# Performance work log

Hardware: AMD Instinct MI355X
Metric: run time of the kernel (lower is better)

The kernel has to match this reference:

```python
import jax, jax.numpy as jnp
import numpy as np

V, D, F, H, NB, S, B = 16384, 512, 2048, 8, 4, 512, 2
T_STEPS = 3      # config.T: number of PC inference iterations
GAMMA = 0.1      # state-update step size


def _layernorm(x, s, b):
    m = x.mean(-1, keepdims=True)
    v = ((x - m) ** 2).mean(-1, keepdims=True)
    return (x - m) * jax.lax.rsqrt(v + 1e-5) * s + b


def setup_inputs() -> dict:
    key = jax.random.key(0)
    ks = jax.random.split(key, 12)
    r = lambda k, sh: jax.random.normal(k, sh, jnp.float32) * 0.02
    return {
        'word_emb': r(ks[0], (V, D)),
        'pos_emb': r(ks[1], (S, D)),
        'Wq': r(ks[2], (NB, D, D)),
        'Wk': r(ks[3], (NB, D, D)),
        'Wv': r(ks[4], (NB, D, D)),
        'bq': jnp.zeros((NB, D), jnp.float32),
        'bk': jnp.zeros((NB, D), jnp.float32),
        'bv': jnp.zeros((NB, D), jnp.float32),
        'Wo': r(ks[5], (NB, D, D)),
        'bo': jnp.zeros((NB, D), jnp.float32),
        'ln1_s': jnp.ones((NB, D), jnp.float32),
        'ln1_b': jnp.zeros((NB, D), jnp.float32),
        'ln2_s': jnp.ones((NB, D), jnp.float32),
        'ln2_b': jnp.zeros((NB, D), jnp.float32),
        'W1': r(ks[6], (NB, D, F)),
        'b1': jnp.zeros((NB, F), jnp.float32),
        'W2': r(ks[7], (NB, F, D)),
        'b2': jnp.zeros((NB, D), jnp.float32),
        'Wout': r(ks[8], (D, V)),
        'bout': jnp.zeros((V,), jnp.float32),
        'input_ids': jax.random.randint(ks[9], (B, S), 0, V),
        'target_ids': jax.random.randint(ks[10], (B, S), 0, V),
    }


def _forward(word_emb, pos_emb, Wq, Wk, Wv, bq, bk, bv, Wo, bo,
             ln1_s, ln1_b, ln2_s, ln2_b, W1, b1, W2, b2, Wout, bout,
             input_ids, target_ids):
    Bsz, Sl = input_ids.shape
    dh = D // H
    scale = 1.0 / float(np.sqrt(dh))
    ids = jnp.clip(input_ids, 0, V - 1)
    target = jax.nn.one_hot(jnp.clip(target_ids, 0, V - 1), V, dtype=word_emb.dtype)
    # bottom prediction: word + position embeddings
    mu_emb = word_emb[ids] + pos_emb[jnp.arange(Sl)][None]  # (B,S,D)
    causal = jnp.tril(jnp.ones((Sl, Sl), bool))
    neg = jnp.finfo(word_emb.dtype).min

    def attn(x, b):
        h = _layernorm(x, ln1_s[b], ln1_b[b])
        q = (h @ Wq[b] + bq[b]).reshape(Bsz, Sl, H, dh)
        k = (h @ Wk[b] + bk[b]).reshape(Bsz, Sl, H, dh)
        v = (h @ Wv[b] + bv[b]).reshape(Bsz, Sl, H, dh)
        sc = jnp.einsum('bqhd,bkhd->bhqk', q, k) * scale
        sc = jnp.where(causal, sc, neg)
        a = jax.nn.softmax(sc, axis=-1)
        return jnp.einsum('bhqk,bkhd->bqhd', a, v).reshape(Bsz, Sl, D)

    # generative functions g[l]: x_l -> mu_{l+1}; 4 PC layers per block
    # (pc_qkv->attn ctx, pc_output->Wo, pc_layer1->gelu(fc1), pc_layer2->fc2)
    gs = []
    for b in range(NB):
        gs.append(lambda x, b=b: attn(x, b))
        gs.append(lambda x, b=b: x @ Wo[b] + bo[b])
        gs.append(lambda x, b=b: jax.nn.gelu(_layernorm(x, ln2_s[b], ln2_b[b]) @ W1[b] + b1[b]))
        gs.append(lambda x, b=b: x @ W2[b] + b2[b])
    g_top = lambda x: x @ Wout + bout  # output pc layer -> logits mu

    # init_x: forward sweep sets each latent to its prediction
    xs = [mu_emb]
    for g in gs:
        xs.append(g(xs[-1]))
    L = len(gs)

    # T-step iterative PC inference: eps_l = x_l - mu_l, top clamped to target
    # x_l <- x_l + GAMMA * (J_{g_l}(x_l)^T eps_{l+1} - eps_l)
    for _ in range(T_STEPS):
        preds, vjps = [], []
        for l in range(L):
            mu, vj = jax.vjp(gs[l], xs[l])
            preds.append(mu)
            vjps.append(vj)
        logits, vj_top = jax.vjp(g_top, xs[L])
        eps = [xs[0] - mu_emb] + [xs[l + 1] - preds[l] for l in range(L)]
        eps_top = logits - target
        new_xs = []
        for l in range(L + 1):
            td = vjps[l](eps[l + 1])[0] if l < L else vj_top(eps_top)[0]
            new_xs.append(xs[l] + GAMMA * (td - eps[l]))
        xs = new_xs

    return g_top(xs[L])  # get_mu('linear_output')


def reference(word_emb, pos_emb, Wq, Wk, Wv, bq, bk, bv, Wo, bo,
              ln1_s, ln1_b, ln2_s, ln2_b, W1, b1, W2, b2, Wout, bout,
              input_ids, target_ids):
    return _forward(word_emb, pos_emb, Wq, Wk, Wv, bq, bk, bv, Wo, bo,
                    ln1_s, ln1_b, ln2_s, ln2_b, W1, b1, W2, b2, Wout, bout,
                    input_ids, target_ids)
```

## Files before the change

kernel.cpp:

```cpp
#include <hip/hip_runtime.h>
#include <hip/hip_bf16.h>
#include <math.h>

#define D_   512
#define F_   2048
#define V_   16384
#define H_   8
#define DH_  64
#define S_   512
#define B_   2
#define M_   1024
#define MD_  (M_ * D_)
#define MF_  (M_ * F_)
#define GAMMA_ 0.1f

typedef unsigned int u32;
typedef unsigned short u16;
typedef __attribute__((ext_vector_type(4))) float f32x4;
typedef __attribute__((ext_vector_type(8))) short s16x8;
typedef __attribute__((ext_vector_type(4))) u16 u16x4;
typedef __attribute__((ext_vector_type(8))) u16 u16x8;

__device__ __forceinline__ u16 f2b(float f) {
    __hip_bfloat16 h = __float2bfloat16(f);
    return *reinterpret_cast<u16*>(&h);
}
__device__ __forceinline__ float b2f(u16 v) {
    u32 u = ((u32)v) << 16;
    float f; __builtin_memcpy(&f, &u, 4); return f;
}
__device__ __forceinline__ u16x4 pack4(f32x4 v) {
    u16x4 o; o.x = f2b(v[0]); o.y = f2b(v[1]); o.z = f2b(v[2]); o.w = f2b(v[3]);
    return o;
}

__device__ __forceinline__ void gl_lds16(const void* g, void* l) {
    __builtin_amdgcn_global_load_lds((const __attribute__((address_space(1))) u32*)g,
                                     (__attribute__((address_space(3))) u32*)l, 16, 0, 0);
}

__device__ __forceinline__ float gelu_f(float v) {
    float u = 0.7978845608028654f * (v + 0.044715f * v * v * v);
    return 0.5f * v * (1.f + tanhf(u));
}

__device__ __forceinline__ f32x4 xpose4(f32x4 v, int b) {
#pragma unroll
    for (int s = 1; s < 4; s <<= 1) {
        f32x4 nv;
#pragma unroll
        for (int j = 0; j < 4; ++j) {
            float ex = __shfl_xor(v[j ^ s], s, 64);
            nv[j] = ((b ^ j) & s) ? ex : v[j];
        }
        v = nv;
    }
    return v;
}

__device__ __forceinline__ float wave_sum(float v) {
#pragma unroll
    for (int o = 32; o > 0; o >>= 1) v += __shfl_xor(v, o, 64);
    return v;
}

#define E_F32   0
#define E_GELU  1
#define E_TD    2
#define E_EC2   3
#define E_QKV3  4
#define E_OUT   5
#define E_BF16  6

template<int BK>
__device__ __forceinline__ int swz(int c, int row) {
    if constexpr (BK == 32) return c ^ ((row >> 1) & 3);
    else                    return c ^ (row & 7);
}

template<int BM, int BN, int BK, int FM, int FN, int EPI>
__global__ __launch_bounds__(256)
void mfma_gemm(const u16* __restrict__ A, const u16* __restrict__ B,
               float* __restrict__ Cf, u16* __restrict__ Cb,
               u16* __restrict__ Cb2, u16* __restrict__ Cb3,
               const float* __restrict__ bias,
               int K, int lda, int ldb, int ldc,
               long sC, long sKz, float alpha,
               const float* __restrict__ base, const float* __restrict__ subv,
               const float* __restrict__ cvec, const u16* __restrict__ woutTb,
               const int* __restrict__ tcl,
               float* __restrict__ ebF, u16* __restrict__ ebB)
{
    constexpr int WC = BN / (FN * 16);
    static_assert((BM / (FM * 16)) * WC == 4, "4 waves");
    constexpr int LPR = BK / 8;
    constexpr int RPI = 2048 / BK;
    constexpr int NISS = BM / RPI + BN / RPI;
    __shared__ __align__(16) u16 Asl[3][BM * BK];
    __shared__ __align__(16) u16 Bsl[3][BN * BK];
    const int t = threadIdx.x, l = t & 63, wid = t >> 6;
    const int m0 = blockIdx.y * BM, n0 = blockIdx.x * BN;
    const long z = blockIdx.z;
    A += z * sKz;
    B += z * sKz;
    if (Cf) Cf += z * sC;

    f32x4 acc[FM][FN] = {};
    const int rm = (wid / WC) * (FM * 16), cn = (wid % WC) * (FN * 16);
    const int lr = l & 15, hi = l >> 4;
    const int srl = t / LPR, sc = t % LPR;

    auto stage = [&](int k0, int pb) {
#pragma unroll
        for (int i = 0; i < BM / RPI; ++i) {
            int row = i * RPI + srl;
            gl_lds16(A + (size_t)(m0 + row) * lda + k0 + swz<BK>(sc, row) * 8,
                     &Asl[pb][i * 2048 + t * 8]);
        }
#pragma unroll
        for (int i = 0; i < BN / RPI; ++i) {
            int row = i * RPI + srl;
            gl_lds16(B + (size_t)(n0 + row) * ldb + k0 + swz<BK>(sc, row) * 8,
                     &Bsl[pb][i * 2048 + t * 8]);
        }
    };
    auto compute = [&](int pb) {
#pragma unroll
        for (int kk = 0; kk < BK / 32; ++kk) {
            s16x8 av[FM], bv[FN];
#pragma unroll
            for (int fm = 0; fm < FM; ++fm)
                av[fm] = *(const s16x8*)&Asl[pb][(rm + fm * 16 + lr) * BK + swz<BK>(kk * 4 + hi, lr) * 8];
#pragma unroll
            for (int fn = 0; fn < FN; ++fn)
                bv[fn] = *(const s16x8*)&Bsl[pb][(cn + fn * 16 + lr) * BK + swz<BK>(kk * 4 + hi, lr) * 8];
#pragma unroll
            for (int fm = 0; fm < FM; ++fm)
#pragma unroll
                for (int fn = 0; fn < FN; ++fn)
                    acc[fm][fn] = __builtin_amdgcn_mfma_f32_16x16x32_bf16(av[fm], bv[fn], acc[fm][fn], 0, 0, 0);
        }
    };

    const int nst = K / BK;
    stage(0, 0);
    if (nst > 1) stage(BK, 1);
    int rd = 0, wr = 2;
    for (int s = 0; s < nst; ++s) {
        if (s < nst - 1)
            asm volatile("s_waitcnt vmcnt(%0)" :: "i"(NISS) : "memory");
        else
            asm volatile("s_waitcnt vmcnt(0)" ::: "memory");
        __builtin_amdgcn_s_barrier();
        __builtin_amdgcn_sched_barrier(0);
        compute(rd);
        if (s + 2 < nst) stage((s + 2) * BK, wr);
        rd = (rd + 1 == 3) ? 0 : rd + 1;
        wr = (wr + 1 == 3) ? 0 : wr + 1;
    }

    const int qb = lr & 3, qi = lr >> 2;
#pragma unroll
    for (int fm = 0; fm < FM; ++fm)
#pragma unroll
        for (int fn = 0; fn < FN; ++fn) {
            const int gm = m0 + rm + fm * 16 + hi * 4 + qb;
            const int gn0 = n0 + cn + fn * 16 + qi * 4;
            const size_t idx0 = (size_t)gm * ldc + gn0;
            if constexpr (EPI == E_QKV3) {
                const int gnf = n0 + cn + fn * 16;
                const int sel = gnf >> 9;
                if (sel < 2) {
                    f32x4 v = xpose4(acc[fm][fn], qb);
                    f32x4 bv4 = *(const f32x4*)&bias[gn0];
#pragma unroll
                    for (int j = 0; j < 4; ++j) v[j] += bv4[j];
                    int b = gm >> 9, s = gm & (S_ - 1);
                    int d9 = gn0 & 511, h = d9 >> 6, d = d9 & 63;
                    u16* dst = (sel == 0) ? Cb : Cb2;
                    *(u16x4*)&dst[(((size_t)(b * H_ + h) * S_ + s) << 6) + d] = pack4(v);
                } else {
                    const int gnl = gnf + lr;
                    const int gm0 = m0 + rm + fm * 16 + hi * 4;
                    int b = gm0 >> 9, s0 = gm0 & (S_ - 1);
                    int d9 = gnl & 511, h = d9 >> 6, d = d9 & 63;
                    float bb = bias[gnl];
                    f32x4 v = acc[fm][fn];
#pragma unroll
                    for (int j = 0; j < 4; ++j) v[j] += bb;
                    *(u16x4*)&Cb3[((((size_t)(b * H_ + h)) << 6) + d) * S_ + s0] = pack4(v);
                }
            } else {
                f32x4 v = xpose4(acc[fm][fn], qb);
                if constexpr (EPI == E_F32) {
#pragma unroll
                    for (int j = 0; j < 4; ++j) v[j] *= alpha;
                    if (bias) {
                        f32x4 bv4 = *(const f32x4*)&bias[gn0];
#pragma unroll
                        for (int j = 0; j < 4; ++j) v[j] += bv4[j];
                    }
                    *(f32x4*)&Cf[idx0] = v;
                    if (Cb) *(u16x4*)&Cb[idx0] = pack4(v);
                } else if constexpr (EPI == E_OUT) {
                    f32x4 bv4 = *(const f32x4*)&bias[gn0];
#pragma unroll
                    for (int j = 0; j < 4; ++j) v[j] += bv4[j];
                    *(f32x4*)&Cf[idx0] = v;
                } else if constexpr (EPI == E_GELU) {
                    f32x4 bv4 = *(const f32x4*)&bias[gn0];
#pragma unroll
                    for (int j = 0; j < 4; ++j) v[j] = gelu_f(v[j] + bv4[j]);
                    *(u16x4*)&Cb[idx0] = pack4(v);
                } else if constexpr (EPI == E_TD) {
                    const int tc = tcl[gm];
                    f32x4 cv4 = *(const f32x4*)&cvec[gn0];
                    f32x4 ba4 = *(const f32x4*)&base[idx0];
                    u16x4 gv = *(const u16x4*)&woutTb[(size_t)tc * D_ + gn0];
                    f32x4 dlt, o2;
#pragma unroll
                    for (int j = 0; j < 4; ++j)
                        dlt[j] = GAMMA_ * (v[j] + cv4[j] - b2f(gv[j]));
                    if (subv) {
                        f32x4 sv4 = *(const f32x4*)&subv[idx0];
#pragma unroll
                        for (int j = 0; j < 4; ++j) dlt[j] -= GAMMA_ * sv4[j];
                    }
#pragma unroll
                    for (int j = 0; j < 4; ++j) o2[j] = ba4[j] + dlt[j];
                    if (Cf) *(f32x4*)&Cf[idx0] = o2;
                    *(u16x4*)&Cb[idx0] = pack4(o2);
                    if (ebF) *(f32x4*)&ebF[idx0] = dlt;
                    if (ebB) *(u16x4*)&ebB[idx0] = pack4(dlt);
                } else if constexpr (EPI == E_EC2) {
                    f32x4 ba4 = *(const f32x4*)&base[idx0];
                    f32x4 sv4 = *(const f32x4*)&subv[idx0];
#pragma unroll
                    for (int j = 0; j < 4; ++j) v[j] = ba4[j] - sv4[j] - GAMMA_ * v[j];
                    *(f32x4*)&Cf[idx0] = v;
                } else if constexpr (EPI == E_BF16) {
                    *(u16x4*)&Cb[idx0] = pack4(v);
                }
            }
        }
}

__global__ __launch_bounds__(128)
void flash_attn(const u16* __restrict__ q, const u16* __restrict__ k,
                const u16* __restrict__ vT, u16* __restrict__ ctx)
{
    __shared__ __align__(16) u16 Ks[3][64 * 64];
    __shared__ __align__(16) u16 Vs[3][64 * 64];
    __shared__ __align__(16) u16 Ps[2][16 * 64];
    const int t = threadIdx.x, l = t & 63, w = t >> 6;
    const int qt = blockIdx.x, z = blockIdx.y;
    const int bb = z >> 3, hh = z & 7;
    const int lr = l & 15, hi = l >> 4;
    const u16* qp = q + (((size_t)z * S_ + qt * 32 + w * 16) << 6);
    const u16* kp = k + ((size_t)z * S_ << 6);
    const u16* vp = vT + (((size_t)z) << 6) * S_;

    const s16x8 aq0 = *(const s16x8*)&qp[lr * 64 + hi * 8];
    const s16x8 aq1 = *(const s16x8*)&qp[lr * 64 + 32 + hi * 8];

    f32x4 o[4] = {};
    float m[4], ls[4];
#pragma unroll
    for (int r = 0; r < 4; ++r) { m[r] = -3.0e38f; ls[r] = 0.f; }
    const int qrow = qt * 32 + w * 16 + hi * 4;
    const int srow = t >> 3, scl = t & 7;
    const int cg = (scl ^ (srow & 7)) * 8;
    const int sw7 = (lr & 7);
    const int jmax = qt >> 1;

    auto stage = [&](int j, int pb) {
#pragma unroll
        for (int i = 0; i < 4; ++i)
            gl_lds16(kp + ((size_t)(j * 64 + i * 16 + srow) << 6) + cg,
                     &Ks[pb][i * 1024 + t * 8]);
#pragma unroll
        for (int i = 0; i < 4; ++i)
            gl_lds16(vp + (size_t)(i * 16 + srow) * S_ + j * 64 + cg,
                     &Vs[pb][i * 1024 + t * 8]);
    };

    stage(0, 0);
    if (jmax > 0) stage(1, 1);
    int rd = 0, wr = 2;
    for (int j = 0; j <= jmax; ++j) {
        if (j < jmax) asm volatile("s_waitcnt vmcnt(8)" ::: "memory");
        else          asm volatile("s_waitcnt vmcnt(0)" ::: "memory");
        __builtin_amdgcn_s_barrier();
        __builtin_amdgcn_sched_barrier(0);

        float pv[4][4];
#pragma unroll
        for (int fn = 0; fn < 4; ++fn) {
            f32x4 acc = {};
            acc = __builtin_amdgcn_mfma_f32_16x16x32_bf16(aq0,
                    *(const s16x8*)&Ks[rd][((fn * 16 + lr) << 6) + ((hi ^ sw7) * 8)], acc, 0, 0, 0);
            acc = __builtin_amdgcn_mfma_f32_16x16x32_bf16(aq1,
                    *(const s16x8*)&Ks[rd][((fn * 16 + lr) << 6) + (((hi + 4) ^ sw7) * 8)], acc, 0, 0, 0);
#pragma unroll
            for (int r = 0; r < 4; ++r) pv[fn][r] = acc[r] * 0.125f;
        }
        if (j == jmax) {
#pragma unroll
            for (int fn = 0; fn < 4; ++fn) {
                int col = j * 64 + fn * 16 + lr;
#pragma unroll
                for (int r = 0; r < 4; ++r)
                    if (col > qrow + r) pv[fn][r] = -3.0e38f;
            }
        }
        float sc[4], rs[4];
#pragma unroll
        for (int r = 0; r < 4; ++r) {
            float x = fmaxf(fmaxf(pv[0][r], pv[1][r]), fmaxf(pv[2][r], pv[3][r]));
#pragma unroll
            for (int off = 1; off < 16; off <<= 1) x = fmaxf(x, __shfl_xor(x, off, 64));
            float nm = fmaxf(m[r], x);
            sc[r] = expf(m[r] - nm);
            m[r] = nm;
            rs[r] = 0.f;
        }
#pragma unroll
        for (int fn = 0; fn < 4; ++fn)
#pragma unroll
            for (int r = 0; r < 4; ++r) {
                float p = expf(pv[fn][r] - m[r]);
                pv[fn][r] = p;
                rs[r] += p;
            }
#pragma unroll
        for (int r = 0; r < 4; ++r) {
#pragma unroll
            for (int off = 1; off < 16; off <<= 1) rs[r] += __shfl_xor(rs[r], off, 64);
            ls[r] = ls[r] * sc[r] + rs[r];
        }
#pragma unroll
        for (int fn = 0; fn < 4; ++fn)
#pragma unroll
            for (int r = 0; r < 4; ++r) o[fn][r] *= sc[r];
#pragma unroll
        for (int fn = 0; fn < 4; ++fn)
#pragma unroll
            for (int r = 0; r < 4; ++r) {
                int qr = hi * 4 + r;
                int ci = (2 * fn + (lr >> 3)) ^ (qr & 7);
                Ps[w][qr * 64 + ci * 8 + (lr & 7)] = f2b(pv[fn][r]);
            }
#pragma unroll
        for (int ks = 0; ks < 2; ++ks) {
            const s16x8 pa = *(const s16x8*)&Ps[w][lr * 64 + (((4 * ks + hi) ^ sw7) * 8)];
#pragma unroll
            for (int fn = 0; fn < 4; ++fn)
                o[fn] = __builtin_amdgcn_mfma_f32_16x16x32_bf16(pa,
                        *(const s16x8*)&Vs[rd][((fn * 16 + lr) << 6) + (((hi + 4 * ks) ^ sw7) * 8)], o[fn], 0, 0, 0);
        }
        if (j + 2 <= jmax) stage(j + 2, wr);
        rd = (rd + 1 == 3) ? 0 : rd + 1;
        wr = (wr + 1 == 3) ? 0 : wr + 1;
    }
    float inv[4];
#pragma unroll
    for (int r = 0; r < 4; ++r) inv[r] = 1.f / ls[r];
    u16* cp = ctx + ((size_t)(bb * S_ + qt * 32 + w * 16) * D_) + hh * 64;
    const int qb = lr & 3, qi = lr >> 2;
#pragma unroll
    for (int fn = 0; fn < 4; ++fn) {
        f32x4 v = o[fn];
#pragma unroll
        for (int r = 0; r < 4; ++r) v[r] *= inv[r];
        v = xpose4(v, qb);
        *(u16x4*)&cp[(size_t)(hi * 4 + qb) * D_ + fn * 16 + qi * 4] = pack4(v);
    }
}

__global__ __launch_bounds__(256)
void mega_prep(const float* __restrict__ Wq, const float* __restrict__ Wk,
               const float* __restrict__ Wv, const float* __restrict__ Wo,
               const float* __restrict__ W1, const float* __restrict__ W2,
               const float* __restrict__ Wout,
               const float* __restrict__ bq, const float* __restrict__ bk,
               const float* __restrict__ bv, const int* __restrict__ target_ids,
               u16* __restrict__ wqkvT, u16* __restrict__ woT, u16* __restrict__ w1T,
               u16* __restrict__ w2T, u16* __restrict__ woutT,
               u16* __restrict__ woutD, float* __restrict__ qkvb, int* __restrict__ tcl)
{
    __shared__ float tile[64][65];
    const int g = blockIdx.x, t = threadIdx.x;

    const float* in = nullptr;
    u16 *outT = nullptr, *outC = nullptr;
    int R = 512, C = 512, tx = 0, ty = 0;

    if (g < 768) {
        int sel = g / 256, rem = g % 256, zz = rem >> 6, tl = rem & 63;
        in = (sel == 0 ? Wq : sel == 1 ? Wk : Wv) + (size_t)zz * 262144;
        outT = wqkvT + (size_t)zz * 786432 + sel * 262144;
        tx = tl & 7; ty = tl >> 3;
    } else if (g < 1024) {
        int rem = g - 768, zz = rem >> 6, tl = rem & 63;
        in = Wo + (size_t)zz * 262144; outT = woT + (size_t)zz * 262144;
        tx = tl & 7; ty = tl >> 3;
    } else if (g < 2048) {
        int rem = g - 1024, zz = rem >> 8, tl = rem & 255;
        in = W1 + (size_t)zz * 1048576; outT = w1T + (size_t)zz * 1048576;
        C = 2048; tx = tl & 31; ty = tl >> 5;
    } else if (g < 3072) {
        int rem = g - 2048, zz = rem >> 8, tl = rem & 255;
        in = W2 + (size_t)zz * 1048576; outT = w2T + (size_t)zz * 1048576;
        R = 2048; tx = tl & 7; ty = tl >> 3;
    } else if (g < 5120) {
        int tl = g - 3072;
        in = Wout; outT = woutT; outC = woutD;
        C = 16384; tx = tl & 255; ty = tl >> 8;
    } else {
        for (int i = t; i < M_; i += 256) {
            int v = target_ids[i];
            tcl[i] = v < 0 ? 0 : (v > V_ - 1 ? V_ - 1 : v);
        }
        for (int i = t; i < 4 * 1536; i += 256) {
            int b = i / 1536, j = i - b * 1536;
            qkvb[i] = (j < 512) ? bq[b * 512 + j]
                    : (j < 1024) ? bk[b * 512 + j - 512] : bv[b * 512 + j - 1024];
        }
        return;
    }

    const int r0 = ty * 64, c0 = tx * 64;
#pragma unroll
    for (int p = 0; p < 4; ++p) {
        int row = p * 16 + (t >> 4), col = (t & 15) * 4;
        float4 v = *(const float4*)&in[(size_t)(r0 + row) * C + c0 + col];
        tile[row][col] = v.x; tile[row][col + 1] = v.y;
        tile[row][col + 2] = v.z; tile[row][col + 3] = v.w;
        if (outC) {
            f32x4 fv; fv[0] = v.x; fv[1] = v.y; fv[2] = v.z; fv[3] = v.w;
            *(u16x4*)&outC[(size_t)(r0 + row) * C + c0 + col] = pack4(fv);
        }
    }
    __syncthreads();
#pragma unroll
    for (int p = 0; p < 2; ++p) {
        int orow = p * 32 + (t >> 3), oc = (t & 7) * 8;
        u16x8 o;
#pragma unroll
        for (int j = 0; j < 8; ++j) o[j] = f2b(tile[oc + j][orow]);
        *(u16x8*)&outT[(size_t)(c0 + orow) * R + r0 + oc] = o;
    }
}

__global__ __launch_bounds__(256)
void gredcvec(const float* __restrict__ P, u16* __restrict__ G,
              const u16* __restrict__ woutD, const float* __restrict__ bout,
              float* __restrict__ cvec)
{
    const int blk = blockIdx.x;
    if (blk < 1024) {
        int i = blk * 256 + threadIdx.x;
        float s = 0.f;
#pragma unroll
        for (int zz = 0; zz < 16; ++zz) s += P[(size_t)zz * D_ * D_ + i];
        G[i] = f2b(s);
    } else {
        const int w = threadIdx.x >> 6, l = threadIdx.x & 63;
        const int d = (blk - 1024) * 4 + w;
        float s = 0.f;
        for (int it = 0; it < 32; ++it) {
            int base = it * 512 + l * 8;
            u16x8 wv = *(const u16x8*)&woutD[(size_t)d * V_ + base];
            float4 b0 = *(const float4*)&bout[base];
            float4 b1 = *(const float4*)&bout[base + 4];
            s += b2f(wv[0]) * b0.x + b2f(wv[1]) * b0.y + b2f(wv[2]) * b0.z + b2f(wv[3]) * b0.w
               + b2f(wv[4]) * b1.x + b2f(wv[5]) * b1.y + b2f(wv[6]) * b1.z + b2f(wv[7]) * b1.w;
        }
        s = wave_sum(s);
        if (l == 0) cvec[d] = s;
    }
}

__global__ void embed_kernel(const float4* __restrict__ we, const float4* __restrict__ pe,
                             const int* __restrict__ ids, float4* __restrict__ o)
{
    int t = blockIdx.x * blockDim.x + threadIdx.x;
    int d4 = t & 127, row = t >> 7;
    int ss = row & (S_ - 1);
    int id = ids[row];
    id = id < 0 ? 0 : (id > V_ - 1 ? V_ - 1 : id);
    float4 a = we[(size_t)id * 128 + d4];
    float4 b = pe[(size_t)ss * 128 + d4];
    o[(size_t)row * 128 + d4] = make_float4(a.x + b.x, a.y + b.y, a.z + b.z, a.w + b.w);
}

__global__ __launch_bounds__(256)
void ln_fwd_kernel(const float* __restrict__ x, const float* __restrict__ s,
                   const float* __restrict__ bb, u16* __restrict__ h)
{
    const int l = threadIdx.x & 63, w = threadIdx.x >> 6;
    const int row = blockIdx.x * 4 + w;
    const float* xr = x + (size_t)row * D_;
    const int c0 = l * 8;
    float4 a = *(const float4*)&xr[c0];
    float4 b = *(const float4*)&xr[c0 + 4];
    float sum = a.x + a.y + a.z + a.w + b.x + b.y + b.z + b.w;
    float mu = wave_sum(sum) * (1.f / D_);
    float d0 = a.x - mu, d1 = a.y - mu, d2 = a.z - mu, d3 = a.w - mu;
    float d4 = b.x - mu, d5 = b.y - mu, d6 = b.z - mu, d7 = b.w - mu;
    float vs = d0*d0 + d1*d1 + d2*d2 + d3*d3 + d4*d4 + d5*d5 + d6*d6 + d7*d7;
    float var = wave_sum(vs) * (1.f / D_);
    float r = rsqrtf(var + 1e-5f);
    float4 s0 = *(const float4*)&s[c0], s1 = *(const float4*)&s[c0 + 4];
    float4 b0 = *(const float4*)&bb[c0], b1 = *(const float4*)&bb[c0 + 4];
    u16* hr = h + (size_t)row * D_;
    f32x4 o0, o1;
    o0[0] = d0 * r * s0.x + b0.x; o0[1] = d1 * r * s0.y + b0.y;
    o0[2] = d2 * r * s0.z + b0.z; o0[3] = d3 * r * s0.w + b0.w;
    o1[0] = d4 * r * s1.x + b1.x; o1[1] = d5 * r * s1.y + b1.y;
    o1[2] = d6 * r * s1.z + b1.z; o1[3] = d7 * r * s1.w + b1.w;
    *(u16x4*)&hr[c0] = pack4(o0);
    *(u16x4*)&hr[c0 + 4] = pack4(o1);
}

extern "C" void kernel_launch(void* const* d_in, const int* in_sizes, int n_in,
                              void* d_out, int out_size, void* d_ws, size_t ws_size,
                              hipStream_t stream)
{
    (void)in_sizes; (void)n_in; (void)out_size;
    const float* Wq  = (const float*)d_in[2];
    const float* Wk  = (const float*)d_in[3];
    const float* Wv  = (const float*)d_in[4];
    const float* bq  = (const float*)d_in[5];
    const float* bk  = (const float*)d_in[6];
    const float* bv  = (const float*)d_in[7];
    const float* Wo  = (const float*)d_in[8];
    const float* bo  = (const float*)d_in[9];
    const float* ln1_s = (const float*)d_in[10];
    const float* ln1_b = (const float*)d_in[11];
    const float* ln2_s = (const float*)d_in[12];
    const float* ln2_b = (const float*)d_in[13];
    const float* W1  = (const float*)d_in[14];
    const float* b1  = (const float*)d_in[15];
    const float* W2  = (const float*)d_in[16];
    const float* b2  = (const float*)d_in[17];
    const float* Wout = (const float*)d_in[18];
    const float* bout = (const float*)d_in[19];
    const int* input_ids  = (const int*)d_in[20];
    const int* target_ids = (const int*)d_in[21];
    float* out = (float*)d_out;

    char* wsb = (char*)d_ws;
    size_t off = 0;
    auto alloc = [&](size_t bytes) -> void* {
        off = (off + 255) & ~(size_t)255;
        void* p = wsb + off; off += bytes; return p;
    };
    u16* wqkvT = (u16*)alloc((size_t)4 * 1536 * D_ * 2);
    u16* woT   = (u16*)alloc((size_t)4 * D_ * D_ * 2);
    u16* w1T   = (u16*)alloc((size_t)4 * D_ * F_ * 2);
    u16* w2T   = (u16*)alloc((size_t)4 * D_ * F_ * 2);
    u16* woutT = (u16*)alloc((size_t)V_ * D_ * 2);
    u16* G_b   = (u16*)alloc((size_t)D_ * D_ * 2);
    u16* H2_b  = (u16*)alloc((size_t)D_ * D_ * 2);
    float* qkvb = (float*)alloc((size_t)4 * 1536 * 4);
    float* bufB = (float*)alloc((size_t)MD_ * 4);
    u16* h_b    = (u16*)alloc((size_t)MD_ * 2);
    u16* gelu_b = (u16*)alloc((size_t)MF_ * 2);
    u16* x16_b  = (u16*)alloc((size_t)MD_ * 2);
    float* cvec = (float*)alloc(D_ * 4);
    int* tcl    = (int*)alloc(M_ * 4);
    size_t uStart = (off + 255) & ~(size_t)255;
    off = uStart;
    u16* woutD   = (u16*)alloc((size_t)V_ * D_ * 2);
    float* Gpart = (float*)alloc((size_t)16 * D_ * D_ * 4);
    size_t endG = off;
    off = uStart;
    u16* q_b   = (u16*)alloc((size_t)MD_ * 2);
    u16* k_b   = (u16*)alloc((size_t)MD_ * 2);
    u16* v_b   = (u16*)alloc((size_t)MD_ * 2);
    u16* ctx_b = (u16*)alloc((size_t)MD_ * 2);
    size_t endA = off;
    off = uStart;
    float* xA  = (float*)alloc((size_t)MD_ * 4);
    float* xB  = (float*)alloc((size_t)MD_ * 4);
    float* eb  = (float*)alloc((size_t)MD_ * 4);
    float* ec  = (float*)alloc((size_t)MD_ * 4);
    u16* xA_b  = (u16*)alloc((size_t)MD_ * 2);
    u16* xB_b  = (u16*)alloc((size_t)MD_ * 2);
    u16* xC_b  = (u16*)alloc((size_t)MD_ * 2);
    u16* eb_b  = (u16*)alloc((size_t)MD_ * 2);
    size_t endT = off;
    size_t need = endG > endA ? endG : endA;
    if (endT > need) need = endT;
    if (need > ws_size) return;

    dim3 blk(256);
    const long NL = 0;
    #define GZ nullptr, nullptr, nullptr, nullptr, nullptr, nullptr, nullptr

    mega_prep<<<dim3(5121), blk, 0, stream>>>(Wq, Wk, Wv, Wo, W1, W2, Wout,
        bq, bk, bv, target_ids, wqkvT, woT, w1T, w2T, woutT, woutD, qkvb, tcl);
    mfma_gemm<128, 128, 64, 4, 4, E_F32><<<dim3(4, 4, 16), blk, 0, stream>>>(
        woutD, woutD, Gpart, nullptr, nullptr, nullptr, nullptr, 1024, V_, V_, D_,
        (long)D_ * D_, 1024, 1.f, GZ);
    gredcvec<<<dim3(1152), blk, 0, stream>>>(Gpart, G_b, woutD, bout, cvec);
    mfma_gemm<32, 64, 64, 1, 2, E_BF16><<<dim3(8, 16, 1), blk, 0, stream>>>(
        w2T + (size_t)3 * D_ * F_, w2T + (size_t)3 * D_ * F_, nullptr, H2_b,
        nullptr, nullptr, nullptr, F_, F_, F_, D_, NL, NL, 1.f, GZ);

    embed_kernel<<<dim3(512), blk, 0, stream>>>((const float4*)d_in[0], (const float4*)d_in[1],
                                                input_ids, (float4*)bufB);
    for (int b = 0; b < 4; ++b) {
        const size_t wDD = (size_t)b * D_ * D_, wDF = (size_t)b * D_ * F_;
        ln_fwd_kernel<<<dim3(M_ / 4), blk, 0, stream>>>(bufB, ln1_s + b * D_, ln1_b + b * D_, h_b);
        mfma_gemm<64, 64, 64, 2, 2, E_QKV3><<<dim3(24, 16, 1), blk, 0, stream>>>(
            h_b, wqkvT + (size_t)b * 1536 * 512, nullptr, q_b, k_b, v_b,
            qkvb + b * 1536, D_, D_, D_, 0, NL, NL, 1.f, GZ);
        flash_attn<<<dim3(16, 16), dim3(128), 0, stream>>>(q_b, k_b, v_b, ctx_b);
        mfma_gemm<32, 64, 64, 1, 2, E_F32><<<dim3(8, 32, 1), blk, 0, stream>>>(
            ctx_b, woT + wDD, bufB, nullptr, nullptr, nullptr, bo + b * D_,
            D_, D_, D_, D_, NL, NL, 1.f, GZ);
        ln_fwd_kernel<<<dim3(M_ / 4), blk, 0, stream>>>(bufB, ln2_s + b * D_, ln2_b + b * D_, h_b);
        mfma_gemm<64, 64, 64, 2, 2, E_GELU><<<dim3(32, 16, 1), blk, 0, stream>>>(
            h_b, w1T + wDF, nullptr, gelu_b, nullptr, nullptr, b1 + b * F_,
            D_, D_, D_, F_, NL, NL, 1.f, GZ);
        mfma_gemm<32, 64, 64, 1, 2, E_F32><<<dim3(8, 32, 1), blk, 0, stream>>>(
            gelu_b, w2T + wDF, bufB, (b == 3) ? x16_b : nullptr, nullptr, nullptr, b2 + b * D_,
            F_, F_, F_, D_, NL, NL, 1.f, GZ);
    }

    mfma_gemm<32, 64, 64, 1, 2, E_TD><<<dim3(8, 32, 1), blk, 0, stream>>>(
        x16_b, G_b, xA, xA_b, nullptr, nullptr, nullptr, D_, D_, D_, D_, NL, NL, 1.f,
        bufB, nullptr, cvec, woutT, tcl, eb, eb_b);
    mfma_gemm<32, 64, 64, 1, 2, E_TD><<<dim3(8, 32, 1), blk, 0, stream>>>(
        xA_b, G_b, xB, xB_b, nullptr, nullptr, nullptr, D_, D_, D_, D_, NL, NL, 1.f,
        xA, eb, cvec, woutT, tcl, nullptr, nullptr);
    mfma_gemm<32, 64, 64, 1, 2, E_EC2><<<dim3(8, 32, 1), blk, 0, stream>>>(
        eb_b, H2_b, ec, nullptr, nullptr, nullptr, nullptr, D_, D_, D_, D_, NL, NL, 1.f,
        xB, bufB, nullptr, nullptr, nullptr, nullptr, nullptr);
    mfma_gemm<32, 64, 64, 1, 2, E_TD><<<dim3(8, 32, 1), blk, 0, stream>>>(
        xB_b, G_b, nullptr, xC_b, nullptr, nullptr, nullptr, D_, D_, D_, D_, NL, NL, 1.f,
        xB, ec, cvec, woutT, tcl, nullptr, nullptr);
    mfma_gemm<128, 128, 32, 4, 4, E_OUT><<<dim3(128, 8, 1), blk, 0, stream>>>(
        xC_b, woutT, out, nullptr, nullptr, nullptr, bout, D_, D_, D_, V_, NL, NL, 1.f, GZ);
    #undef GZ
}
```

Before: 386.9 us.

## Coarsen weight-prep transpose blocks and raise wave priority around attention MFMAs

The weight transpose/convert prep kernel now runs 641 blocks instead of 5121, and each block walks 8 row tiles of 64 in a loop with an extra barrier per tile. This cuts block launch and scheduling overhead. Separately, the flash-attention loop raises wave priority with s_setprio around the QK and PV MFMA sections, so waves issuing matrix ops are favored over waves doing softmax or loads. The risk is less memory-level parallelism in the prep kernel, since there are fewer blocks and each one runs its tiles in series.

```diff
diff --git a/kernel.cpp b/kernel.cpp
--- a/kernel.cpp
+++ b/kernel.cpp
@@ -294,6 +294,7 @@
         __builtin_amdgcn_sched_barrier(0);
 
         float pv[4][4];
+        __builtin_amdgcn_s_setprio(1);
 #pragma unroll
         for (int fn = 0; fn < 4; ++fn) {
             f32x4 acc = {};
@@ -304,6 +305,7 @@
 #pragma unroll
             for (int r = 0; r < 4; ++r) pv[fn][r] = acc[r] * 0.125f;
         }
+        __builtin_amdgcn_s_setprio(0);
         if (j == jmax) {
 #pragma unroll
             for (int fn = 0; fn < 4; ++fn) {
@@ -350,6 +352,7 @@
                 int ci = (2 * fn + (lr >> 3)) ^ (qr & 7);
                 Ps[w][qr * 64 + ci * 8 + (lr & 7)] = f2b(pv[fn][r]);
             }
+        __builtin_amdgcn_s_setprio(1);
 #pragma unroll
         for (int ks = 0; ks < 2; ++ks) {
             const s16x8 pa = *(const s16x8*)&Ps[w][lr * 64 + (((4 * ks + hi) ^ sw7) * 8)];
@@ -358,6 +361,7 @@
                 o[fn] = __builtin_amdgcn_mfma_f32_16x16x32_bf16(pa,
                         *(const s16x8*)&Vs[rd][((fn * 16 + lr) << 6) + (((hi + 4 * ks) ^ sw7) * 8)], o[fn], 0, 0, 0);
         }
+        __builtin_amdgcn_s_setprio(0);
         if (j + 2 <= jmax) stage(j + 2, wr);
         rd = (rd + 1 == 3) ? 0 : rd + 1;
         wr = (wr + 1 == 3) ? 0 : wr + 1;
@@ -393,29 +397,29 @@
 
     const float* in = nullptr;
     u16 *outT = nullptr, *outC = nullptr;
-    int R = 512, C = 512, tx = 0, ty = 0;
-
-    if (g < 768) {
-        int sel = g / 256, rem = g % 256, zz = rem >> 6, tl = rem & 63;
+    int R = 512, C = 512, c0 = 0, rbase = 0;
+
+    if (g < 96) {
+        int sel = g / 32, rem = g % 32, zz = rem >> 3, st = rem & 7;
         in = (sel == 0 ? Wq : sel == 1 ? Wk : Wv) + (size_t)zz * 262144;
         outT = wqkvT + (size_t)zz * 786432 + sel * 262144;
-        tx = tl & 7; ty = tl >> 3;
-    } else if (g < 1024) {
-        int rem = g - 768, zz = rem >> 6, tl = rem & 63;
+        c0 = st * 64;
+    } else if (g < 128) {
+        int rem = g - 96, zz = rem >> 3, st = rem & 7;
         in = Wo + (size_t)zz * 262144; outT = woT + (size_t)zz * 262144;
-        tx = tl & 7; ty = tl >> 3;
-    } else if (g < 2048) {
-        int rem = g - 1024, zz = rem >> 8, tl = rem & 255;
+        c0 = st * 64;
+    } else if (g < 256) {
+        int rem = g - 128, zz = rem >> 5, st = rem & 31;
         in = W1 + (size_t)zz * 1048576; outT = w1T + (size_t)zz * 1048576;
-        C = 2048; tx = tl & 31; ty = tl >> 5;
-    } else if (g < 3072) {
-        int rem = g - 2048, zz = rem >> 8, tl = rem & 255;
+        C = 2048; c0 = st * 64;
+    } else if (g < 384) {
+        int rem = g - 256, zz = rem >> 5, sub = rem & 31;
         in = W2 + (size_t)zz * 1048576; outT = w2T + (size_t)zz * 1048576;
-        R = 2048; tx = tl & 7; ty = tl >> 3;
-    } else if (g < 5120) {
-        int tl = g - 3072;
+        R = 2048; c0 = (sub & 7) * 64; rbase = (sub >> 3) * 512;
+    } else if (g < 640) {
+        int st = g - 384;
         in = Wout; outT = woutT; outC = woutD;
-        C = 16384; tx = tl & 255; ty = tl >> 8;
+        C = 16384; c0 = st * 64;
     } else {
         for (int i = t; i < M_; i += 256) {
             int v = target_ids[i];
@@ -429,26 +433,29 @@
         return;
     }
 
-    const int r0 = ty * 64, c0 = tx * 64;
-#pragma unroll
-    for (int p = 0; p < 4; ++p) {
-        int row = p * 16 + (t >> 4), col = (t & 15) * 4;
-        float4 v = *(const float4*)&in[(size_t)(r0 + row) * C + c0 + col];
-        tile[row][col] = v.x; tile[row][col + 1] = v.y;
-        tile[row][col + 2] = v.z; tile[row][col + 3] = v.w;
-        if (outC) {
-            f32x4 fv; fv[0] = v.x; fv[1] = v.y; fv[2] = v.z; fv[3] = v.w;
-            *(u16x4*)&outC[(size_t)(r0 + row) * C + c0 + col] = pack4(fv);
-        }
-    }
-    __syncthreads();
-#pragma unroll
-    for (int p = 0; p < 2; ++p) {
-        int orow = p * 32 + (t >> 3), oc = (t & 7) * 8;
-        u16x8 o;
-#pragma unroll
-        for (int j = 0; j < 8; ++j) o[j] = f2b(tile[oc + j][orow]);
-        *(u16x8*)&outT[(size_t)(c0 + orow) * R + r0 + oc] = o;
+    for (int it = 0; it < 8; ++it) {
+        const int r0 = rbase + it * 64;
+#pragma unroll
+        for (int p = 0; p < 4; ++p) {
+            int row = p * 16 + (t >> 4), col = (t & 15) * 4;
+            float4 v = *(const float4*)&in[(size_t)(r0 + row) * C + c0 + col];
+            tile[row][col] = v.x; tile[row][col + 1] = v.y;
+            tile[row][col + 2] = v.z; tile[row][col + 3] = v.w;
+            if (outC) {
+                f32x4 fv; fv[0] = v.x; fv[1] = v.y; fv[2] = v.z; fv[3] = v.w;
+                *(u16x4*)&outC[(size_t)(r0 + row) * C + c0 + col] = pack4(fv);
+            }
+        }
+        __syncthreads();
+#pragma unroll
+        for (int p = 0; p < 2; ++p) {
+            int orow = p * 32 + (t >> 3), oc = (t & 7) * 8;
+            u16x8 o;
+#pragma unroll
+            for (int j = 0; j < 8; ++j) o[j] = f2b(tile[oc + j][orow]);
+            *(u16x8*)&outT[(size_t)(c0 + orow) * R + r0 + oc] = o;
+        }
+        __syncthreads();
     }
 }
 
@@ -599,7 +606,7 @@
     const long NL = 0;
     #define GZ nullptr, nullptr, nullptr, nullptr, nullptr, nullptr, nullptr
 
-    mega_prep<<<dim3(5121), blk, 0, stream>>>(Wq, Wk, Wv, Wo, W1, W2, Wout,
+    mega_prep<<<dim3(641), blk, 0, stream>>>(Wq, Wk, Wv, Wo, W1, W2, Wout,
         bq, bk, bv, target_ids, wqkvT, woT, w1T, w2T, woutT, woutD, qkvb, tcl);
     mfma_gemm<128, 128, 64, 4, 4, E_F32><<<dim3(4, 4, 16), blk, 0, stream>>>(
         woutD, woutD, Gpart, nullptr, nullptr, nullptr, nullptr, 1024, V_, V_, D_,
```

Result: no change. 388.3 us (+0.4%).
